# Optimization experiments

Measured on AMD Instinct MI355X. Metric: run time of the kernel, lower is better.

## Reference

```python
import jax, jax.numpy as jnp
import numpy as np

IN_CH, OUT_CH, KH, KW = 512, 512, 3, 3
LR_MULT = 1.0
WEIGHT_SCALE = LR_MULT / np.sqrt(IN_CH * KH * KW)


def setup_inputs() -> dict:
    key = jax.random.key(0)
    k1, k2, k3 = jax.random.split(key, 3)
    x = jax.random.normal(k1, (16, IN_CH, 32, 32), dtype=jnp.float32)
    s = jax.random.normal(k2, (16, IN_CH), dtype=jnp.float32)
    weight = jax.random.normal(k3, (OUT_CH, IN_CH, KH, KW), dtype=jnp.float32) / LR_MULT
    return {"x": x, "s": s, "weight": weight}


def reference(x, s, weight):
    B, Cin, H, Wd = x.shape
    Cout = weight.shape[0]
    W = weight * WEIGHT_SCALE                          # [Cout, Cin, kH, kW]
    # per-sample modulation: [B, Cout, Cin, kH, kW]
    Wm = s[:, None, :, None, None] * W[None]
    # demodulation: normalize each (b, out_channel) filter
    sigma = jnp.sqrt(jnp.sum(Wm ** 2, axis=(-3, -2, -1), keepdims=True) + 1e-8)
    Wm = Wm / sigma
    # grouped conv with groups = B
    x_g = x.reshape(1, B * Cin, H, Wd)
    W_g = Wm.reshape(B * Cout, Cin, KH, KW)
    out = jax.lax.conv_general_dilated(
        x_g, W_g,
        window_strides=(1, 1),
        padding="SAME",
        rhs_dilation=(1, 1),
        feature_group_count=B,
        dimension_numbers=("NCHW", "OIHW", "NCHW"),
    )
    return out.reshape(B, Cout, out.shape[-2], out.shape[-1])
```

## Files before the change

kernel.cpp:

```cpp
#include <hip/hip_runtime.h>
#include <hip/hip_bf16.h>


typedef __attribute__((ext_vector_type(4))) float f32x4;
typedef __attribute__((ext_vector_type(8))) short bf16x8;

#define NB    16
#define CIN   512
#define COUT  512
#define KTOT  4608
#define NPIX  (NB * 32 * 32)
#define KTILES 72
#define BUFBYTES 49152

#define WAITV12() asm volatile("s_waitcnt vmcnt(12)" ::: "memory")
#define WAITV0()  asm volatile("s_waitcnt vmcnt(0)" ::: "memory")
#define FENCE()   asm volatile("" ::: "memory")
#define BAR()     { FENCE(); __builtin_amdgcn_s_barrier(); FENCE(); }

__device__ __forceinline__ void gload_lds16(const void* g, void* l) {
  __builtin_amdgcn_global_load_lds(
      (__attribute__((address_space(1))) void*)(g),
      (__attribute__((address_space(3))) void*)(l), 16, 0, 0);
}

__global__ __launch_bounds__(256) void pack_w_kernel(
    const float* __restrict__ w, __hip_bfloat16* __restrict__ wB,
    float* __restrict__ wsq) {
  const int idx = blockIdx.x * 256 + threadIdx.x;
  const int o = idx >> 9, ci = idx & 511;
  const float* wp = w + (size_t)idx * 9;
  const float WSCALE = 0.014731391274719739f;
  float sum = 0.f;
#pragma unroll
  for (int t = 0; t < 9; ++t) {
    float v = wp[t] * WSCALE;
    sum += v * v;
    wB[(size_t)o * KTOT + t * 512 + ci] = __float2bfloat16(v);
  }
  wsq[idx] = sum;
}

__global__ __launch_bounds__(256) void calc_rsig_kernel(
    const float* __restrict__ s, const float* __restrict__ wsq,
    float* __restrict__ rsig) {
  const int wid = blockIdx.x * 4 + (threadIdx.x >> 6);
  const int lane = threadIdx.x & 63;
  const int b = wid >> 9, o = wid & 511;
  const float* sp = s + b * 512;
  const float* wp = wsq + o * 512;
  float sum = 0.f;
#pragma unroll
  for (int i = 0; i < 8; ++i) {
    float sv = sp[lane + i * 64];
    sum += sv * sv * wp[lane + i * 64];
  }
#pragma unroll
  for (int off = 32; off > 0; off >>= 1) sum += __shfl_down(sum, off, 64);
  if (lane == 0) rsig[wid] = 1.0f / sqrtf(sum + 1e-8f);
}

__global__ __launch_bounds__(256) void modulate_kernel(
    const float* __restrict__ x, const float* __restrict__ s,
    __hip_bfloat16* __restrict__ xpad) {
  const int by = blockIdx.x;
  const int b = by >> 5, y = by & 31;
  __shared__ __attribute__((aligned(16))) __hip_bfloat16 tile[32][72];
  const int tid = threadIdx.x;
  const int xc = tid & 31;
  const int cr0 = tid >> 5;
  const float* xrow = x + ((size_t)b * 512 * 32 + y) * 32;
  const float* sb = s + b * 512;
  __hip_bfloat16* orow = xpad + (size_t)((b * 34 + y + 1) * 34) * 512;

  for (int ci0 = 0; ci0 < 512; ci0 += 64) {
#pragma unroll
    for (int r = 0; r < 8; ++r) {
      const int cir = r * 8 + cr0;
      const int ci = ci0 + cir;
      float v = xrow[(size_t)ci * 1024 + xc] * sb[ci];
      tile[xc][cir] = __float2bfloat16(v);
    }
    __syncthreads();
    const int xcw = tid >> 3, vec = tid & 7;
    bf16x8 v = *(const bf16x8*)&tile[xcw][vec * 8];
    *(bf16x8*)(orow + (size_t)(xcw + 1) * 512 + ci0 + vec * 8) = v;
    __syncthreads();
  }
}

__global__ __launch_bounds__(256, 1) void conv_gemm_kernel(
    const __hip_bfloat16* __restrict__ wB,
    const __hip_bfloat16* __restrict__ xpad,
    const float* __restrict__ rsig,
    float* __restrict__ out) {
  extern __shared__ __attribute__((aligned(16))) char ldsc[];

  const int tid = threadIdx.x;
  const int wv = tid >> 6, lane = tid & 63, l15 = lane & 15;
  const int bo0 = blockIdx.y << 7;
  const int bp0 = blockIdx.x << 8;
  const int bimg = blockIdx.x >> 2;
  const int wr = wv >> 1, wc = wv & 1;

  int gA[4];
#pragma unroll
  for (int r = 0; r < 4; ++r) {
    const int c = r * 256 + tid, row = c >> 3, sc = (c & 7) ^ (row & 7);
    gA[r] = (bo0 + row) * KTOT + sc * 8;
  }
  int gB[8];
#pragma unroll
  for (int r = 0; r < 8; ++r) {
    const int c = r * 256 + tid, row = c >> 3, sc = (c & 7) ^ (row & 7);
    const int p = bp0 + row, b = p >> 10, rem = p & 1023, y = rem >> 5,
              xx = rem & 31;
    gB[r] = ((b * 34 + y) * 34 + xx) * 512 + sc * 8;
  }

  auto stage = [&](int kt) {
    char* base = ldsc + (kt % 3) * BUFBYTES;
    const int tap = kt >> 3;
    const int xoff = (tap + 31 * (tap / 3)) * 512 + ((kt & 7) << 6);
#pragma unroll
    for (int r = 0; r < 4; ++r)
      gload_lds16(wB + (size_t)(gA[r] + (kt << 6)),
                  base + (r * 256 + tid) * 16);
#pragma unroll
    for (int r = 0; r < 8; ++r)
      gload_lds16(xpad + (size_t)(gB[r] + xoff),
                  base + 16384 + (r * 256 + tid) * 16);
  };

  f32x4 acc[4][8];
#pragma unroll
  for (int mi = 0; mi < 4; ++mi)
#pragma unroll
    for (int ni = 0; ni < 8; ++ni) acc[mi][ni] = f32x4{0.f, 0.f, 0.f, 0.f};

  const int kb0 = (lane >> 4) << 4;

  stage(0);
  stage(1);

#pragma unroll 1
  for (int kt = 0; kt < KTILES; ++kt) {
    if (kt < KTILES - 1) { WAITV12(); } else { WAITV0(); }
    BAR();
    if (kt + 2 < KTILES) stage(kt + 2);

    const char* bufA = ldsc + (kt % 3) * BUFBYTES;
    const char* bufB = bufA + 16384;

    bf16x8 af[4][2];
#pragma unroll
    for (int mi = 0; mi < 4; ++mi) {
      const int row = (wr << 6) + (mi << 4) + l15;
      const int swz = (row & 7) << 4;
      af[mi][0] = *(const bf16x8*)(bufA + row * 128 + (kb0 ^ swz));
      af[mi][1] = *(const bf16x8*)(bufA + row * 128 + ((64 | kb0) ^ swz));
    }
    {
      bf16x8 bv[8];
#pragma unroll
      for (int ni = 0; ni < 8; ++ni) {
        const int row = (wc << 7) + (ni << 4) + l15;
        bv[ni] = *(const bf16x8*)(bufB + row * 128 + (kb0 ^ ((row & 7) << 4)));
      }
#pragma unroll
      for (int mi = 0; mi < 4; ++mi)
#pragma unroll
        for (int ni = 0; ni < 8; ++ni)
          acc[mi][ni] = __builtin_amdgcn_mfma_f32_16x16x32_bf16(
              af[mi][0], bv[ni], acc[mi][ni], 0, 0, 0);
    }
    {
      bf16x8 bv[8];
#pragma unroll
      for (int ni = 0; ni < 8; ++ni) {
        const int row = (wc << 7) + (ni << 4) + l15;
        bv[ni] = *(const bf16x8*)(bufB + row * 128 +
                                  ((64 | kb0) ^ ((row & 7) << 4)));
      }
#pragma unroll
      for (int mi = 0; mi < 4; ++mi)
#pragma unroll
        for (int ni = 0; ni < 8; ++ni)
          acc[mi][ni] = __builtin_amdgcn_mfma_f32_16x16x32_bf16(
              af[mi][1], bv[ni], acc[mi][ni], 0, 0, 0);
    }
  }

#pragma unroll
  for (int mi = 0; mi < 4; ++mi) {
    const int o = bo0 + (wr << 6) + (mi << 4) + ((lane >> 4) << 2);
    const f32x4 rs = *(const f32x4*)(rsig + (bimg << 9) + o);
#pragma unroll
    for (int ni = 0; ni < 8; ++ni) {
      const int p = bp0 + (wc << 7) + (ni << 4) + l15;
      const int prem = p & 1023;
#pragma unroll
      for (int r = 0; r < 4; ++r)
        out[((size_t)(bimg << 9) + o + r) * 1024 + prem] =
            acc[mi][ni][r] * rs[r];
    }
  }
}

extern "C" void kernel_launch(void* const* d_in, const int* in_sizes, int n_in,
                              void* d_out, int out_size, void* d_ws,
                              size_t ws_size, hipStream_t stream) {
  const float* x = (const float*)d_in[0];
  const float* s = (const float*)d_in[1];
  const float* w = (const float*)d_in[2];
  float* out = (float*)d_out;

  char* ws = (char*)d_ws;
  const size_t xpad_bytes = (size_t)NB * 34 * 34 * 512 * 2;
  const size_t wB_bytes = (size_t)COUT * KTOT * 2;
  const size_t wsq_bytes = (size_t)COUT * CIN * 4;
  __hip_bfloat16* xpad = (__hip_bfloat16*)ws;
  __hip_bfloat16* wB = (__hip_bfloat16*)(ws + xpad_bytes);
  float* wsq = (float*)(ws + xpad_bytes + wB_bytes);
  float* rsig = (float*)(ws + xpad_bytes + wB_bytes + wsq_bytes);

  const int lds_bytes = 3 * BUFBYTES;
  hipFuncSetAttribute((const void*)conv_gemm_kernel,
                      hipFuncAttributeMaxDynamicSharedMemorySize, lds_bytes);

  hipMemsetAsync(xpad, 0, xpad_bytes, stream);
  pack_w_kernel<<<(COUT * CIN) / 256, 256, 0, stream>>>(w, wB, wsq);
  modulate_kernel<<<NB * 32, 256, 0, stream>>>(x, s, xpad);
  calc_rsig_kernel<<<(NB * COUT) / 4, 256, 0, stream>>>(s, wsq, rsig);
  conv_gemm_kernel<<<dim3(NPIX / 256, COUT / 128), 256, lds_bytes, stream>>>(
      wB, xpad, rsig, out);
}
```

Before: 112.3 us.

## Split K across wave pairs with 512-thread blocks and LDS reduction

The GEMM block grows from 4 to 8 waves. Each pair of waves splits the 64-wide K tile in half, so every wave issues half the MFMAs per tile, and the partial accumulators are summed through LDS at the end. Loads per thread are halved to match, and MFMA sections are wrapped in s_setprio. The goal is more waves in flight to hide LDS and global latency, at the cost of an extra reduction pass through LDS and more barrier participants.

```diff
diff --git a/kernel.cpp b/kernel.cpp
--- a/kernel.cpp
+++ b/kernel.cpp
@@ -13,10 +13,10 @@
 #define KTILES 72
 #define BUFBYTES 49152
 
-#define WAITV12() asm volatile("s_waitcnt vmcnt(12)" ::: "memory")
-#define WAITV0()  asm volatile("s_waitcnt vmcnt(0)" ::: "memory")
-#define FENCE()   asm volatile("" ::: "memory")
-#define BAR()     { FENCE(); __builtin_amdgcn_s_barrier(); FENCE(); }
+#define WAITV6() asm volatile("s_waitcnt vmcnt(6)" ::: "memory")
+#define WAITV0() asm volatile("s_waitcnt vmcnt(0)" ::: "memory")
+#define FENCE()  asm volatile("" ::: "memory")
+#define BAR()    { FENCE(); __builtin_amdgcn_s_barrier(); FENCE(); }
 
 __device__ __forceinline__ void gload_lds16(const void* g, void* l) {
   __builtin_amdgcn_global_load_lds(
@@ -89,7 +89,7 @@
   }
 }
 
-__global__ __launch_bounds__(256, 1) void conv_gemm_kernel(
+__global__ __launch_bounds__(512, 1) void conv_gemm_kernel(
     const __hip_bfloat16* __restrict__ wB,
     const __hip_bfloat16* __restrict__ xpad,
     const float* __restrict__ rsig,
@@ -101,18 +101,18 @@
   const int bo0 = blockIdx.y << 7;
   const int bp0 = blockIdx.x << 8;
   const int bimg = blockIdx.x >> 2;
-  const int wr = wv >> 1, wc = wv & 1;
-
-  int gA[4];
+  const int wr = wv >> 2, wc = (wv >> 1) & 1, wk = wv & 1;
+
+  int gA[2];
+#pragma unroll
+  for (int r = 0; r < 2; ++r) {
+    const int c = r * 512 + tid, row = c >> 3, sc = (c & 7) ^ (row & 7);
+    gA[r] = (bo0 + row) * KTOT + sc * 8;
+  }
+  int gB[4];
 #pragma unroll
   for (int r = 0; r < 4; ++r) {
-    const int c = r * 256 + tid, row = c >> 3, sc = (c & 7) ^ (row & 7);
-    gA[r] = (bo0 + row) * KTOT + sc * 8;
-  }
-  int gB[8];
-#pragma unroll
-  for (int r = 0; r < 8; ++r) {
-    const int c = r * 256 + tid, row = c >> 3, sc = (c & 7) ^ (row & 7);
+    const int c = r * 512 + tid, row = c >> 3, sc = (c & 7) ^ (row & 7);
     const int p = bp0 + row, b = p >> 10, rem = p & 1023, y = rem >> 5,
               xx = rem & 31;
     gB[r] = ((b * 34 + y) * 34 + xx) * 512 + sc * 8;
@@ -123,13 +123,13 @@
     const int tap = kt >> 3;
     const int xoff = (tap + 31 * (tap / 3)) * 512 + ((kt & 7) << 6);
 #pragma unroll
+    for (int r = 0; r < 2; ++r)
+      gload_lds16(wB + (size_t)(gA[r] + (kt << 6)),
+                  base + (r * 512 + tid) * 16);
+#pragma unroll
     for (int r = 0; r < 4; ++r)
-      gload_lds16(wB + (size_t)(gA[r] + (kt << 6)),
-                  base + (r * 256 + tid) * 16);
-#pragma unroll
-    for (int r = 0; r < 8; ++r)
       gload_lds16(xpad + (size_t)(gB[r] + xoff),
-                  base + 16384 + (r * 256 + tid) * 16);
+                  base + 16384 + (r * 512 + tid) * 16);
   };
 
   f32x4 acc[4][8];
@@ -138,71 +138,68 @@
 #pragma unroll
     for (int ni = 0; ni < 8; ++ni) acc[mi][ni] = f32x4{0.f, 0.f, 0.f, 0.f};
 
-  const int kb0 = (lane >> 4) << 4;
+  const int kb0 = (wk << 6) | ((lane >> 4) << 4);
 
   stage(0);
   stage(1);
 
 #pragma unroll 1
   for (int kt = 0; kt < KTILES; ++kt) {
-    if (kt < KTILES - 1) { WAITV12(); } else { WAITV0(); }
+    if (kt < KTILES - 1) { WAITV6(); } else { WAITV0(); }
     BAR();
     if (kt + 2 < KTILES) stage(kt + 2);
 
     const char* bufA = ldsc + (kt % 3) * BUFBYTES;
     const char* bufB = bufA + 16384;
 
-    bf16x8 af[4][2];
+    bf16x8 af[4], bv[8];
 #pragma unroll
     for (int mi = 0; mi < 4; ++mi) {
       const int row = (wr << 6) + (mi << 4) + l15;
-      const int swz = (row & 7) << 4;
-      af[mi][0] = *(const bf16x8*)(bufA + row * 128 + (kb0 ^ swz));
-      af[mi][1] = *(const bf16x8*)(bufA + row * 128 + ((64 | kb0) ^ swz));
-    }
-    {
-      bf16x8 bv[8];
+      af[mi] = *(const bf16x8*)(bufA + row * 128 + (kb0 ^ ((row & 7) << 4)));
+    }
+#pragma unroll
+    for (int ni = 0; ni < 8; ++ni) {
+      const int row = (wc << 7) + (ni << 4) + l15;
+      bv[ni] = *(const bf16x8*)(bufB + row * 128 + (kb0 ^ ((row & 7) << 4)));
+    }
+    __builtin_amdgcn_s_setprio(1);
+#pragma unroll
+    for (int mi = 0; mi < 4; ++mi)
+#pragma unroll
+      for (int ni = 0; ni < 8; ++ni)
+        acc[mi][ni] = __builtin_amdgcn_mfma_f32_16x16x32_bf16(
+            af[mi], bv[ni], acc[mi][ni], 0, 0, 0);
+    __builtin_amdgcn_s_setprio(0);
+  }
+
+  __syncthreads();
+  const int slot = ((wr << 1) | wc) << 15;
+  if (wk) {
+#pragma unroll
+    for (int mi = 0; mi < 4; ++mi)
+#pragma unroll
+      for (int ni = 0; ni < 8; ++ni)
+        *(f32x4*)(ldsc + slot + (((mi << 3) | ni) << 10) + (lane << 4)) =
+            acc[mi][ni];
+  }
+  __syncthreads();
+  if (!wk) {
+#pragma unroll
+    for (int mi = 0; mi < 4; ++mi) {
+      const int o = bo0 + (wr << 6) + (mi << 4) + ((lane >> 4) << 2);
+      const f32x4 rs = *(const f32x4*)(rsig + (bimg << 9) + o);
 #pragma unroll
       for (int ni = 0; ni < 8; ++ni) {
-        const int row = (wc << 7) + (ni << 4) + l15;
-        bv[ni] = *(const bf16x8*)(bufB + row * 128 + (kb0 ^ ((row & 7) << 4)));
+        const f32x4 o4 =
+            *(const f32x4*)(ldsc + slot + (((mi << 3) | ni) << 10) + (lane << 4));
+        const f32x4 a = acc[mi][ni] + o4;
+        const int p = bp0 + (wc << 7) + (ni << 4) + l15;
+        const int prem = p & 1023;
+#pragma unroll
+        for (int r = 0; r < 4; ++r)
+          out[((size_t)(bimg << 9) + o + r) * 1024 + prem] = a[r] * rs[r];
       }
-#pragma unroll
-      for (int mi = 0; mi < 4; ++mi)
-#pragma unroll
-        for (int ni = 0; ni < 8; ++ni)
-          acc[mi][ni] = __builtin_amdgcn_mfma_f32_16x16x32_bf16(
-              af[mi][0], bv[ni], acc[mi][ni], 0, 0, 0);
-    }
-    {
-      bf16x8 bv[8];
-#pragma unroll
-      for (int ni = 0; ni < 8; ++ni) {
-        const int row = (wc << 7) + (ni << 4) + l15;
-        bv[ni] = *(const bf16x8*)(bufB + row * 128 +
-                                  ((64 | kb0) ^ ((row & 7) << 4)));
-      }
-#pragma unroll
-      for (int mi = 0; mi < 4; ++mi)
-#pragma unroll
-        for (int ni = 0; ni < 8; ++ni)
-          acc[mi][ni] = __builtin_amdgcn_mfma_f32_16x16x32_bf16(
-              af[mi][1], bv[ni], acc[mi][ni], 0, 0, 0);
-    }
-  }
-
-#pragma unroll
-  for (int mi = 0; mi < 4; ++mi) {
-    const int o = bo0 + (wr << 6) + (mi << 4) + ((lane >> 4) << 2);
-    const f32x4 rs = *(const f32x4*)(rsig + (bimg << 9) + o);
-#pragma unroll
-    for (int ni = 0; ni < 8; ++ni) {
-      const int p = bp0 + (wc << 7) + (ni << 4) + l15;
-      const int prem = p & 1023;
-#pragma unroll
-      for (int r = 0; r < 4; ++r)
-        out[((size_t)(bimg << 9) + o + r) * 1024 + prem] =
-            acc[mi][ni][r] * rs[r];
     }
   }
 }
@@ -232,6 +229,6 @@
   pack_w_kernel<<<(COUT * CIN) / 256, 256, 0, stream>>>(w, wB, wsq);
   modulate_kernel<<<NB * 32, 256, 0, stream>>>(x, s, xpad);
   calc_rsig_kernel<<<(NB * COUT) / 4, 256, 0, stream>>>(s, wsq, rsig);
-  conv_gemm_kernel<<<dim3(NPIX / 256, COUT / 128), 256, lds_bytes, stream>>>(
+  conv_gemm_kernel<<<dim3(NPIX / 256, COUT / 128), 512, lds_bytes, stream>>>(
       wB, xpad, rsig, out);
 }
```

Result: faster. 103.0 us (-8.2%).
